# Optimization experiments

Hardware: AMD Instinct MI355X
Metric: run time of the kernel (lower is better)

The kernel has to match this reference:

```python
import jax, jax.numpy as jnp
import numpy as np

D = 64       # CNF state dimension
H = 512      # MLP hidden width
B = 8192     # batch


def setup_inputs() -> dict:
    key = jax.random.key(0)
    ks = jax.random.split(key, 8)
    s1 = 1.0 / np.sqrt(D + 1)
    s2 = 1.0 / np.sqrt(H)
    return {
        "t": jax.random.uniform(ks[0], (1,), dtype=jnp.float32),
        "x": jax.random.normal(ks[1], (B, D + 1), dtype=jnp.float32),
        "W1": jax.random.normal(ks[2], (D + 1, H), dtype=jnp.float32) * s1,
        "b1": jnp.zeros((H,), dtype=jnp.float32),
        "W2": jax.random.normal(ks[3], (H, H), dtype=jnp.float32) * s2,
        "b2": jnp.zeros((H,), dtype=jnp.float32),
        "W3": jax.random.normal(ks[4], (H, D), dtype=jnp.float32) * s2,
        "b3": jnp.zeros((D,), dtype=jnp.float32),
    }


def reference(t, x, W1, b1, W2, b2, W3, b3):
    # CNF.forward: strip log-density channel, evaluate vf and its exact divergence.
    xs = x[..., :-1]                      # [B, D]
    tt = t[0]

    def vf_single(xi):                    # xi: [D] -> [D]
        inp = jnp.concatenate([tt[None], xi])          # vf(t*ones, x) with t prepended
        h = jnp.tanh(inp @ W1 + b1)
        h = jnp.tanh(h @ W2 + b2)
        return h @ W3 + b3

    dx = jax.vmap(vf_single)(xs)                        # [B, D]
    # exact divergence: trace of per-sample Jacobian via reverse-mode (matches torch jacrev)
    J = jax.vmap(jax.jacrev(vf_single))(xs)             # [B, D, D]
    div = jnp.trace(J, axis1=-2, axis2=-1)              # [B]
    return jnp.concatenate([dx, div[:, None]], axis=-1) # [B, D+1]
```

## Files before the change

### kernel.cpp

```cpp
#include <hip/hip_runtime.h>

#define HH 512
#define DD 64
#define MROWS 16
#define TPB 256
#define LP 520

typedef unsigned short u16;
typedef short s16x8 __attribute__((ext_vector_type(8)));
typedef float f32x4 __attribute__((ext_vector_type(4)));

#define MFMA16(A,B,C) __builtin_amdgcn_mfma_f32_16x16x32_bf16((A),(B),(C),0,0,0)

#define OFF_W2K  0
#define OFF_EFK  262144
#define OFF_W1F  524288
#define OFF_W3F  557056
#define OFF_Z0B  (589824 * 2)

__device__ __forceinline__ u16 f2bf(float f) {
    unsigned u = __builtin_bit_cast(unsigned, f);
    u += 0x7fffu + ((u >> 16) & 1u);
    return (u16)(u >> 16);
}
__device__ __forceinline__ float bf2f(u16 h) {
    return __builtin_bit_cast(float, (unsigned)h << 16);
}
__device__ __forceinline__ float fast_tanh(float x) {
    float e = __expf(2.0f * x);
    return 1.0f - 2.0f * __builtin_amdgcn_rcpf(e + 1.0f);
}
__device__ __forceinline__ void gll(const u16* g, u16* l) {
    __builtin_amdgcn_global_load_lds(
        (const __attribute__((address_space(1))) unsigned int*)g,
        (__attribute__((address_space(3))) unsigned int*)l, 16, 0, 0);
}
__device__ __forceinline__ void wait_vm4() {
    asm volatile("s_waitcnt vmcnt(4)" ::: "memory");
}
__device__ __forceinline__ void wait_vm0() {
    asm volatile("s_waitcnt vmcnt(0)" ::: "memory");
}
__device__ __forceinline__ void fence_lds_reads() {
    asm volatile("s_waitcnt lgkmcnt(0)" ::: "memory");
}

__global__ __launch_bounds__(256) void precompute(
    const float* __restrict__ t,  const float* __restrict__ W1,
    const float* __restrict__ b1, const float* __restrict__ W2,
    const float* __restrict__ W3, u16* __restrict__ ws16, float* __restrict__ z0)
{
    __shared__ float T[16 * 264 > 256 * 20 ? 16 * 264 : 256 * 20];
    u16* W2K = ws16 + OFF_W2K;
    u16* EFK = ws16 + OFF_EFK;
    u16* W1F = ws16 + OFF_W1F;
    u16* W3F = ws16 + OFF_W3F;

    const int bid = blockIdx.x, tid = threadIdx.x;
    const int lane = tid & 63, wv = tid >> 6;
    const int m16 = lane & 15, q = lane >> 4;

    if (bid < 64) {
        const int nt = bid >> 1, bh = bid & 1;
        const int a0 = nt * 16, b0 = bh * 256;
        s16x8 afh[2], afl[2];
#pragma unroll
        for (int h = 0; h < 2; ++h)
#pragma unroll
            for (int j = 0; j < 8; ++j) {
                int i = h * 32 + q * 8 + j;
                float v = W1[(1 + i) * HH + a0 + m16];
                u16 hi = f2bf(v);
                afh[h][j] = (short)hi;
                afl[h][j] = (short)f2bf(v - bf2f(hi));
            }
#pragma unroll
        for (int bt = 0; bt < 4; ++bt) {
            int bl = wv * 64 + bt * 16;
            s16x8 bfh[2], bfl[2];
#pragma unroll
            for (int h = 0; h < 2; ++h) {
                const float* src = W3 + (b0 + bl + m16) * DD + h * 32 + q * 8;
                float4 p0 = *(const float4*)(src);
                float4 p1 = *(const float4*)(src + 4);
                float vv[8] = {p0.x,p0.y,p0.z,p0.w,p1.x,p1.y,p1.z,p1.w};
#pragma unroll
                for (int j = 0; j < 8; ++j) {
                    u16 hi = f2bf(vv[j]);
                    bfh[h][j] = (short)hi;
                    bfl[h][j] = (short)f2bf(vv[j] - bf2f(hi));
                }
            }
            f32x4 c = {0.f, 0.f, 0.f, 0.f};
#pragma unroll
            for (int h = 0; h < 2; ++h) {
                c = MFMA16(afh[h], bfh[h], c);
                c = MFMA16(afh[h], bfl[h], c);
                c = MFMA16(afl[h], bfh[h], c);
            }
#pragma unroll
            for (int r = 0; r < 4; ++r)
                T[(4 * q + r) * 264 + bl + m16] = c[r];
        }
        __syncthreads();
#pragma unroll
        for (int p = 0; p < 2; ++p) {
            int ksl = p * 4 + wv;
            int al  = m16;
            int blc = ksl * 32 + q * 8;
            const float* w2p = W2 + (a0 + al) * HH + b0 + blc;
            float4 wa = *(const float4*)(w2p), wb = *(const float4*)(w2p + 4);
            const float* glp = T + al * 264 + blc;
            s16x8 o;
            o[0]=(short)f2bf(wa.x*glp[0]); o[1]=(short)f2bf(wa.y*glp[1]);
            o[2]=(short)f2bf(wa.z*glp[2]); o[3]=(short)f2bf(wa.w*glp[3]);
            o[4]=(short)f2bf(wb.x*glp[4]); o[5]=(short)f2bf(wb.y*glp[5]);
            o[6]=(short)f2bf(wb.z*glp[6]); o[7]=(short)f2bf(wb.w*glp[7]);
            *(s16x8*)(EFK + (b0 / 32 + ksl) * 16384 + nt * 512 + lane * 8) = o;
        }
        if (bh == 0 && tid < 128) {
            int ks = tid >> 6, ln = tid & 63;
            int n  = nt * 16 + (ln & 15);
            int k0 = ks * 32 + (ln >> 4) * 8;
            s16x8 o;
#pragma unroll
            for (int j = 0; j < 8; ++j) o[j] = (short)f2bf(W1[(1 + k0 + j) * HH + n]);
            *(s16x8*)(W1F + nt * 1024 + ks * 512 + ln * 8) = o;
        }
    } else if (bid < 128) {
        const int nt = (bid - 64) >> 1, kh = (bid - 64) & 1;
        const int n0 = nt * 16, k0 = kh * 256;
#pragma unroll
        for (int it = 0; it < 4; ++it) {
            int r = (tid >> 2) + it * 64;
            int c = (tid & 3) * 4;
            float4 v = *(const float4*)(W2 + (k0 + r) * HH + n0 + c);
            *(float4*)(T + r * 20 + c) = v;
        }
        __syncthreads();
#pragma unroll
        for (int p = 0; p < 2; ++p) {
            int ksl = p * 4 + wv;
            int kqx = ksl * 32 + q * 8;
            s16x8 o;
#pragma unroll
            for (int j = 0; j < 8; ++j) o[j] = (short)f2bf(T[(kqx + j) * 20 + m16]);
            *(s16x8*)(W2K + (k0 / 32 + ksl) * 16384 + nt * 512 + lane * 8) = o;
        }
    } else if (bid < 136) {
        const int ot = (bid - 128) >> 1, kh = (bid - 128) & 1;
        const int o0 = ot * 16, k0 = kh * 256;
#pragma unroll
        for (int it = 0; it < 4; ++it) {
            int r = (tid >> 2) + it * 64;
            int c = (tid & 3) * 4;
            float4 v = *(const float4*)(W3 + (k0 + r) * DD + o0 + c);
            *(float4*)(T + r * 20 + c) = v;
        }
        __syncthreads();
#pragma unroll
        for (int p = 0; p < 2; ++p) {
            int ksl = p * 4 + wv;
            int kqx = ksl * 32 + q * 8;
            s16x8 o;
#pragma unroll
            for (int j = 0; j < 8; ++j) o[j] = (short)f2bf(T[(kqx + j) * 20 + m16]);
            *(s16x8*)(W3F + ot * 8192 + (k0 / 32 + ksl) * 512 + lane * 8) = o;
        }
    } else {
        for (int n = tid; n < HH; n += 256)
            z0[n] = b1[n] + t[0] * W1[n];
    }
}

__global__ __launch_bounds__(TPB) void cnf_main(
    const float* __restrict__ x,  const u16* __restrict__ ws16,
    const float* __restrict__ z0, const float* __restrict__ b2,
    const float* __restrict__ b3, float* __restrict__ out)
{
    __shared__ u16 h1s[MROWS * LP];
    __shared__ u16 h2s[MROWS * LP];
    __shared__ u16 stg[2][8192];
    __shared__ float z0s[HH];
    __shared__ float b2s[HH];
    __shared__ float b3s[DD];
    __shared__ float divacc[4][MROWS];

    const u16* W2K = ws16 + OFF_W2K;
    const u16* EFK = ws16 + OFF_EFK;
    const u16* W1F = ws16 + OFF_W1F;
    const u16* W3F = ws16 + OFF_W3F;

    const int tid  = threadIdx.x;
    const int lane = tid & 63;
    const int w    = tid >> 6;
    const int m16  = lane & 15;
    const int q    = lane >> 4;
    const int kq   = q * 8;
    const int r0   = blockIdx.x * MROWS;

    u16* xs = h2s;

    for (int idx = tid; idx < MROWS * DD; idx += TPB) {
        int r = idx >> 6, c = idx & 63;
        xs[r * 72 + c] = f2bf(x[(r0 + r) * (DD + 1) + c]);
    }
    for (int n = tid; n < HH; n += TPB) { z0s[n] = z0[n]; b2s[n] = b2[n]; }
    if (tid < DD) b3s[tid] = b3[tid];

    s16x8 b1f[8][2];
#pragma unroll
    for (int j = 0; j < 8; ++j) {
        const u16* bb = W1F + (w * 8 + j) * 1024 + lane * 8;
        b1f[j][0] = *(const s16x8*)(bb);
        b1f[j][1] = *(const s16x8*)(bb + 512);
    }
    __syncthreads();

    {
        s16x8 xa0 = *(const s16x8*)(xs + m16 * 72 + kq);
        s16x8 xa1 = *(const s16x8*)(xs + m16 * 72 + 32 + kq);
#pragma unroll
        for (int j = 0; j < 8; ++j) {
            f32x4 c = {0.f, 0.f, 0.f, 0.f};
            c = MFMA16(xa0, b1f[j][0], c);
            c = MFMA16(xa1, b1f[j][1], c);
            int col = (w * 8 + j) * 16 + m16;
#pragma unroll
            for (int i = 0; i < 4; ++i)
                h1s[(4 * q + i) * LP + col] = f2bf(fast_tanh(c[i] + z0s[col]));
        }
    }
    __syncthreads();

    {
        const u16* abase = h1s + m16 * LP + kq;
        u16* my0 = stg[0] + w * 2048;
        u16* my1 = stg[1] + w * 2048;
#pragma unroll
        for (int g = 0; g < 2; ++g) {
            const u16* wbase = W2K + (g * 16 + w * 4) * 512 + lane * 8;
            fence_lds_reads();
#pragma unroll
            for (int j = 0; j < 4; ++j) gll(wbase + j * 512,         my0 + j * 512);
#pragma unroll
            for (int j = 0; j < 4; ++j) gll(wbase + 16384 + j * 512, my1 + j * 512);
            f32x4 acc[4];
#pragma unroll
            for (int j = 0; j < 4; ++j) acc[j] = f32x4{0.f,0.f,0.f,0.f};
#pragma unroll 4
            for (int c = 0; c < 16; ++c) {
                if (c < 15) wait_vm4(); else wait_vm0();
                u16* sb = (c & 1) ? my1 : my0;
                s16x8 bf0 = *(const s16x8*)(sb +        lane * 8);
                s16x8 bf1 = *(const s16x8*)(sb +  512 + lane * 8);
                s16x8 bf2 = *(const s16x8*)(sb + 1024 + lane * 8);
                s16x8 bf3 = *(const s16x8*)(sb + 1536 + lane * 8);
                s16x8 af  = *(const s16x8*)(abase + c * 32);
                acc[0] = MFMA16(af, bf0, acc[0]);
                acc[1] = MFMA16(af, bf1, acc[1]);
                acc[2] = MFMA16(af, bf2, acc[2]);
                acc[3] = MFMA16(af, bf3, acc[3]);
                if (c < 14) {
                    fence_lds_reads();
                    const u16* src = wbase + (c + 2) * 16384;
#pragma unroll
                    for (int j = 0; j < 4; ++j) gll(src + j * 512, sb + j * 512);
                }
            }
#pragma unroll
            for (int j = 0; j < 4; ++j) {
                int col = (g * 16 + w * 4 + j) * 16 + m16;
#pragma unroll
                for (int i = 0; i < 4; ++i)
                    h2s[(4 * q + i) * LP + col] = f2bf(fast_tanh(acc[j][i] + b2s[col]));
            }
        }
    }
    __syncthreads();

    {
        const u16* ap = h2s + m16 * LP + kq;
        const u16* bp = W3F + w * 8192 + lane * 8;
        s16x8 W3r[4];
#pragma unroll
        for (int k = 0; k < 4; ++k) W3r[k] = *(const s16x8*)(bp + k * 512);
        f32x4 cA = {0.f,0.f,0.f,0.f}, cB = {0.f,0.f,0.f,0.f};
#pragma unroll
        for (int c = 0; c < 16; ++c) {
            s16x8 f = *(const s16x8*)(ap + c * 32);
            const int sl = c & 3;
            if (c & 1) cB = MFMA16(f, W3r[sl], cB);
            else       cA = MFMA16(f, W3r[sl], cA);
            if (c < 12) W3r[sl] = *(const s16x8*)(bp + (c + 4) * 512);
        }
        f32x4 c3 = cA + cB;
        int o = w * 16 + m16;
#pragma unroll
        for (int i = 0; i < 4; ++i)
            out[(r0 + 4 * q + i) * (DD + 1) + o] = c3[i] + b3s[o];
    }

    {
        const u16* abase = h2s + m16 * LP + kq;
        u16* my0 = stg[0] + w * 2048;
        u16* my1 = stg[1] + w * 2048;
        float dpart[4] = {0.f, 0.f, 0.f, 0.f};
#pragma unroll
        for (int g = 0; g < 2; ++g) {
            const u16* ebase = EFK + (g * 16 + w * 4) * 512 + lane * 8;
            fence_lds_reads();
#pragma unroll
            for (int j = 0; j < 4; ++j) gll(ebase + j * 512,         my0 + j * 512);
#pragma unroll
            for (int j = 0; j < 4; ++j) gll(ebase + 16384 + j * 512, my1 + j * 512);
            f32x4 acc[4];
#pragma unroll
            for (int j = 0; j < 4; ++j) acc[j] = f32x4{0.f,0.f,0.f,0.f};
#pragma unroll 4
            for (int c = 0; c < 16; ++c) {
                if (c < 15) wait_vm4(); else wait_vm0();
                u16* sb = (c & 1) ? my1 : my0;
                s16x8 bf0 = *(const s16x8*)(sb +        lane * 8);
                s16x8 bf1 = *(const s16x8*)(sb +  512 + lane * 8);
                s16x8 bf2 = *(const s16x8*)(sb + 1024 + lane * 8);
                s16x8 bf3 = *(const s16x8*)(sb + 1536 + lane * 8);
                s16x8 hf  = *(const s16x8*)(abase + c * 32);
                s16x8 af;
#pragma unroll
                for (int jj = 0; jj < 8; ++jj) {
                    float f = bf2f((u16)hf[jj]);
                    af[jj] = (short)f2bf(1.0f - f * f);
                }
                acc[0] = MFMA16(af, bf0, acc[0]);
                acc[1] = MFMA16(af, bf1, acc[1]);
                acc[2] = MFMA16(af, bf2, acc[2]);
                acc[3] = MFMA16(af, bf3, acc[3]);
                if (c < 14) {
                    fence_lds_reads();
                    const u16* src = ebase + (c + 2) * 16384;
#pragma unroll
                    for (int j = 0; j < 4; ++j) gll(src + j * 512, sb + j * 512);
                }
            }
#pragma unroll
            for (int j = 0; j < 4; ++j) {
                int col = (g * 16 + w * 4 + j) * 16 + m16;
#pragma unroll
                for (int i = 0; i < 4; ++i) {
                    float h1v = bf2f(h1s[(4 * q + i) * LP + col]);
                    dpart[i] += (1.0f - h1v * h1v) * acc[j][i];
                }
            }
        }
#pragma unroll
        for (int i = 0; i < 4; ++i) {
            float v = dpart[i];
            v += __shfl_xor(v, 1, 64);
            v += __shfl_xor(v, 2, 64);
            v += __shfl_xor(v, 4, 64);
            v += __shfl_xor(v, 8, 64);
            if (m16 == 0) divacc[w][4 * q + i] = v;
        }
    }
    __syncthreads();

    if (tid < MROWS) {
        float s = divacc[0][tid] + divacc[1][tid] + divacc[2][tid] + divacc[3][tid];
        out[(r0 + tid) * (DD + 1) + DD] = s;
    }
}

extern "C" void kernel_launch(void* const* d_in, const int* in_sizes, int n_in,
                              void* d_out, int out_size, void* d_ws, size_t ws_size,
                              hipStream_t stream) {
    const float* t  = (const float*)d_in[0];
    const float* x  = (const float*)d_in[1];
    const float* W1 = (const float*)d_in[2];
    const float* b1 = (const float*)d_in[3];
    const float* W2 = (const float*)d_in[4];
    const float* b2 = (const float*)d_in[5];
    const float* W3 = (const float*)d_in[6];
    const float* b3 = (const float*)d_in[7];
    float* out = (float*)d_out;

    u16*   ws16 = (u16*)d_ws;
    float* z0   = (float*)((char*)d_ws + OFF_Z0B);

    precompute<<<137, 256, 0, stream>>>(t, W1, b1, W2, W3, ws16, z0);
    cnf_main<<<8192 / MROWS, TPB, 0, stream>>>(x, ws16, z0, b2, b3, out);
}
```

Before: 104.3 us.

## Process 32 rows per block with 8 waves sharing staged weight tiles

Doubles rows per block to 32 and threads to 512, so each staged W2/EF weight tile feeds two row-tiles of MFMAs. The per-block loop over two column groups goes away, which halves global weight traffic per row. The first W2 tile prefetch is issued before the input load, and the EF prefetch is started before the layer-2 epilogue. The layer-1 tanh derivative is now kept in registers instead of re-read from LDS. In exchange LDS use per block and register pressure both grow, and there are half as many blocks.

```diff
diff --git a/kernel.cpp b/kernel.cpp
--- a/kernel.cpp
+++ b/kernel.cpp
@@ -2,8 +2,8 @@
 
 #define HH 512
 #define DD 64
-#define MROWS 16
-#define TPB 256
+#define MROWS 32
+#define TPB 512
 #define LP 520
 
 typedef unsigned short u16;
@@ -180,11 +180,11 @@
 {
     __shared__ u16 h1s[MROWS * LP];
     __shared__ u16 h2s[MROWS * LP];
-    __shared__ u16 stg[2][8192];
+    __shared__ u16 stg[2][16384];
     __shared__ float z0s[HH];
     __shared__ float b2s[HH];
     __shared__ float b3s[DD];
-    __shared__ float divacc[4][MROWS];
+    __shared__ float divacc[8][MROWS];
 
     const u16* W2K = ws16 + OFF_W2K;
     const u16* EFK = ws16 + OFF_EFK;
@@ -201,87 +201,117 @@
 
     u16* xs = h2s;
 
+#pragma unroll
+    for (int j = 0; j < 4; ++j)
+        gll(W2K + (4 * w + j) * 512 + lane * 8,         stg[0] + w * 2048 + j * 512);
+#pragma unroll
+    for (int j = 0; j < 4; ++j)
+        gll(W2K + 16384 + (4 * w + j) * 512 + lane * 8, stg[1] + w * 2048 + j * 512);
+
     for (int idx = tid; idx < MROWS * DD; idx += TPB) {
         int r = idx >> 6, c = idx & 63;
         xs[r * 72 + c] = f2bf(x[(r0 + r) * (DD + 1) + c]);
     }
-    for (int n = tid; n < HH; n += TPB) { z0s[n] = z0[n]; b2s[n] = b2[n]; }
+    z0s[tid] = z0[tid];
+    b2s[tid] = b2[tid];
     if (tid < DD) b3s[tid] = b3[tid];
 
-    s16x8 b1f[8][2];
-#pragma unroll
-    for (int j = 0; j < 8; ++j) {
-        const u16* bb = W1F + (w * 8 + j) * 1024 + lane * 8;
+    s16x8 b1f[4][2];
+#pragma unroll
+    for (int j = 0; j < 4; ++j) {
+        const u16* bb = W1F + (4 * w + j) * 1024 + lane * 8;
         b1f[j][0] = *(const s16x8*)(bb);
         b1f[j][1] = *(const s16x8*)(bb + 512);
     }
     __syncthreads();
 
+    float d1reg[2][4][4];
+
     {
-        s16x8 xa0 = *(const s16x8*)(xs + m16 * 72 + kq);
-        s16x8 xa1 = *(const s16x8*)(xs + m16 * 72 + 32 + kq);
-#pragma unroll
-        for (int j = 0; j < 8; ++j) {
-            f32x4 c = {0.f, 0.f, 0.f, 0.f};
-            c = MFMA16(xa0, b1f[j][0], c);
-            c = MFMA16(xa1, b1f[j][1], c);
-            int col = (w * 8 + j) * 16 + m16;
+        s16x8 xa[2][2];
+#pragma unroll
+        for (int rt = 0; rt < 2; ++rt) {
+            xa[rt][0] = *(const s16x8*)(xs + (rt * 16 + m16) * 72 + kq);
+            xa[rt][1] = *(const s16x8*)(xs + (rt * 16 + m16) * 72 + 32 + kq);
+        }
+#pragma unroll
+        for (int j = 0; j < 4; ++j) {
+            int col = (4 * w + j) * 16 + m16;
+#pragma unroll
+            for (int rt = 0; rt < 2; ++rt) {
+                f32x4 c = {0.f, 0.f, 0.f, 0.f};
+                c = MFMA16(xa[rt][0], b1f[j][0], c);
+                c = MFMA16(xa[rt][1], b1f[j][1], c);
+#pragma unroll
+                for (int i = 0; i < 4; ++i) {
+                    float hv = fast_tanh(c[i] + z0s[col]);
+                    h1s[(rt * 16 + 4 * q + i) * LP + col] = f2bf(hv);
+                    d1reg[rt][j][i] = 1.0f - hv * hv;
+                }
+            }
+        }
+    }
+    __syncthreads();
+
+    f32x4 acc[2][4];
+#pragma unroll
+    for (int rt = 0; rt < 2; ++rt)
+#pragma unroll
+        for (int j = 0; j < 4; ++j) acc[rt][j] = f32x4{0.f,0.f,0.f,0.f};
+    {
+        const u16* ap0 = h1s + m16 * LP + kq;
+        const u16* ap1 = h1s + (16 + m16) * LP + kq;
+#pragma unroll 4
+        for (int c = 0; c < 16; ++c) {
+            if (c < 15) wait_vm4(); else wait_vm0();
+            u16* sb = stg[c & 1] + w * 2048;
+            s16x8 bf0 = *(const s16x8*)(sb +        lane * 8);
+            s16x8 bf1 = *(const s16x8*)(sb +  512 + lane * 8);
+            s16x8 bf2 = *(const s16x8*)(sb + 1024 + lane * 8);
+            s16x8 bf3 = *(const s16x8*)(sb + 1536 + lane * 8);
+            s16x8 f0  = *(const s16x8*)(ap0 + c * 32);
+            s16x8 f1  = *(const s16x8*)(ap1 + c * 32);
+            acc[0][0] = MFMA16(f0, bf0, acc[0][0]);
+            acc[1][0] = MFMA16(f1, bf0, acc[1][0]);
+            acc[0][1] = MFMA16(f0, bf1, acc[0][1]);
+            acc[1][1] = MFMA16(f1, bf1, acc[1][1]);
+            acc[0][2] = MFMA16(f0, bf2, acc[0][2]);
+            acc[1][2] = MFMA16(f1, bf2, acc[1][2]);
+            acc[0][3] = MFMA16(f0, bf3, acc[0][3]);
+            acc[1][3] = MFMA16(f1, bf3, acc[1][3]);
+            if (c < 14) {
+                fence_lds_reads();
+                const u16* src = W2K + (c + 2) * 16384 + 4 * w * 512 + lane * 8;
+#pragma unroll
+                for (int j = 0; j < 4; ++j) gll(src + j * 512, sb + j * 512);
+            }
+        }
+    }
+
+    fence_lds_reads();
+#pragma unroll
+    for (int j = 0; j < 4; ++j)
+        gll(EFK + (4 * w + j) * 512 + lane * 8,         stg[0] + w * 2048 + j * 512);
+#pragma unroll
+    for (int j = 0; j < 4; ++j)
+        gll(EFK + 16384 + (4 * w + j) * 512 + lane * 8, stg[1] + w * 2048 + j * 512);
+
+#pragma unroll
+    for (int j = 0; j < 4; ++j) {
+        int col = (4 * w + j) * 16 + m16;
+#pragma unroll
+        for (int rt = 0; rt < 2; ++rt)
 #pragma unroll
             for (int i = 0; i < 4; ++i)
-                h1s[(4 * q + i) * LP + col] = f2bf(fast_tanh(c[i] + z0s[col]));
-        }
+                h2s[(rt * 16 + 4 * q + i) * LP + col] =
+                    f2bf(fast_tanh(acc[rt][j][i] + b2s[col]));
     }
     __syncthreads();
 
     {
-        const u16* abase = h1s + m16 * LP + kq;
-        u16* my0 = stg[0] + w * 2048;
-        u16* my1 = stg[1] + w * 2048;
-#pragma unroll
-        for (int g = 0; g < 2; ++g) {
-            const u16* wbase = W2K + (g * 16 + w * 4) * 512 + lane * 8;
-            fence_lds_reads();
-#pragma unroll
-            for (int j = 0; j < 4; ++j) gll(wbase + j * 512,         my0 + j * 512);
-#pragma unroll
-            for (int j = 0; j < 4; ++j) gll(wbase + 16384 + j * 512, my1 + j * 512);
-            f32x4 acc[4];
-#pragma unroll
-            for (int j = 0; j < 4; ++j) acc[j] = f32x4{0.f,0.f,0.f,0.f};
-#pragma unroll 4
-            for (int c = 0; c < 16; ++c) {
-                if (c < 15) wait_vm4(); else wait_vm0();
-                u16* sb = (c & 1) ? my1 : my0;
-                s16x8 bf0 = *(const s16x8*)(sb +        lane * 8);
-                s16x8 bf1 = *(const s16x8*)(sb +  512 + lane * 8);
-                s16x8 bf2 = *(const s16x8*)(sb + 1024 + lane * 8);
-                s16x8 bf3 = *(const s16x8*)(sb + 1536 + lane * 8);
-                s16x8 af  = *(const s16x8*)(abase + c * 32);
-                acc[0] = MFMA16(af, bf0, acc[0]);
-                acc[1] = MFMA16(af, bf1, acc[1]);
-                acc[2] = MFMA16(af, bf2, acc[2]);
-                acc[3] = MFMA16(af, bf3, acc[3]);
-                if (c < 14) {
-                    fence_lds_reads();
-                    const u16* src = wbase + (c + 2) * 16384;
-#pragma unroll
-                    for (int j = 0; j < 4; ++j) gll(src + j * 512, sb + j * 512);
-                }
-            }
-#pragma unroll
-            for (int j = 0; j < 4; ++j) {
-                int col = (g * 16 + w * 4 + j) * 16 + m16;
-#pragma unroll
-                for (int i = 0; i < 4; ++i)
-                    h2s[(4 * q + i) * LP + col] = f2bf(fast_tanh(acc[j][i] + b2s[col]));
-            }
-        }
-    }
-    __syncthreads();
-
-    {
-        const u16* ap = h2s + m16 * LP + kq;
-        const u16* bp = W3F + w * 8192 + lane * 8;
+        const int rowt = w >> 2, ot = w & 3;
+        const u16* ap = h2s + (rowt * 16 + m16) * LP + kq;
+        const u16* bp = W3F + ot * 8192 + lane * 8;
         s16x8 W3r[4];
 #pragma unroll
         for (int k = 0; k < 4; ++k) W3r[k] = *(const s16x8*)(bp + k * 512);
@@ -295,78 +325,74 @@
             if (c < 12) W3r[sl] = *(const s16x8*)(bp + (c + 4) * 512);
         }
         f32x4 c3 = cA + cB;
-        int o = w * 16 + m16;
+        int o = ot * 16 + m16;
 #pragma unroll
         for (int i = 0; i < 4; ++i)
-            out[(r0 + 4 * q + i) * (DD + 1) + o] = c3[i] + b3s[o];
+            out[(r0 + rowt * 16 + 4 * q + i) * (DD + 1) + o] = c3[i] + b3s[o];
     }
 
     {
-        const u16* abase = h2s + m16 * LP + kq;
-        u16* my0 = stg[0] + w * 2048;
-        u16* my1 = stg[1] + w * 2048;
-        float dpart[4] = {0.f, 0.f, 0.f, 0.f};
-#pragma unroll
-        for (int g = 0; g < 2; ++g) {
-            const u16* ebase = EFK + (g * 16 + w * 4) * 512 + lane * 8;
-            fence_lds_reads();
-#pragma unroll
-            for (int j = 0; j < 4; ++j) gll(ebase + j * 512,         my0 + j * 512);
-#pragma unroll
-            for (int j = 0; j < 4; ++j) gll(ebase + 16384 + j * 512, my1 + j * 512);
-            f32x4 acc[4];
-#pragma unroll
-            for (int j = 0; j < 4; ++j) acc[j] = f32x4{0.f,0.f,0.f,0.f};
+        f32x4 g[2][4];
+#pragma unroll
+        for (int rt = 0; rt < 2; ++rt)
+#pragma unroll
+            for (int j = 0; j < 4; ++j) g[rt][j] = f32x4{0.f,0.f,0.f,0.f};
+        const u16* ap0 = h2s + m16 * LP + kq;
+        const u16* ap1 = h2s + (16 + m16) * LP + kq;
 #pragma unroll 4
-            for (int c = 0; c < 16; ++c) {
-                if (c < 15) wait_vm4(); else wait_vm0();
-                u16* sb = (c & 1) ? my1 : my0;
-                s16x8 bf0 = *(const s16x8*)(sb +        lane * 8);
-                s16x8 bf1 = *(const s16x8*)(sb +  512 + lane * 8);
-                s16x8 bf2 = *(const s16x8*)(sb + 1024 + lane * 8);
-                s16x8 bf3 = *(const s16x8*)(sb + 1536 + lane * 8);
-                s16x8 hf  = *(const s16x8*)(abase + c * 32);
-                s16x8 af;
-#pragma unroll
-                for (int jj = 0; jj < 8; ++jj) {
-                    float f = bf2f((u16)hf[jj]);
-                    af[jj] = (short)f2bf(1.0f - f * f);
-                }
-                acc[0] = MFMA16(af, bf0, acc[0]);
-                acc[1] = MFMA16(af, bf1, acc[1]);
-                acc[2] = MFMA16(af, bf2, acc[2]);
-                acc[3] = MFMA16(af, bf3, acc[3]);
-                if (c < 14) {
-                    fence_lds_reads();
-                    const u16* src = ebase + (c + 2) * 16384;
-#pragma unroll
-                    for (int j = 0; j < 4; ++j) gll(src + j * 512, sb + j * 512);
-                }
-            }
-#pragma unroll
-            for (int j = 0; j < 4; ++j) {
-                int col = (g * 16 + w * 4 + j) * 16 + m16;
-#pragma unroll
-                for (int i = 0; i < 4; ++i) {
-                    float h1v = bf2f(h1s[(4 * q + i) * LP + col]);
-                    dpart[i] += (1.0f - h1v * h1v) * acc[j][i];
-                }
-            }
-        }
-#pragma unroll
-        for (int i = 0; i < 4; ++i) {
-            float v = dpart[i];
-            v += __shfl_xor(v, 1, 64);
-            v += __shfl_xor(v, 2, 64);
-            v += __shfl_xor(v, 4, 64);
-            v += __shfl_xor(v, 8, 64);
-            if (m16 == 0) divacc[w][4 * q + i] = v;
-        }
+        for (int c = 0; c < 16; ++c) {
+            if (c < 15) wait_vm4(); else wait_vm0();
+            u16* sb = stg[c & 1] + w * 2048;
+            s16x8 ef0 = *(const s16x8*)(sb +        lane * 8);
+            s16x8 ef1 = *(const s16x8*)(sb +  512 + lane * 8);
+            s16x8 ef2 = *(const s16x8*)(sb + 1024 + lane * 8);
+            s16x8 ef3 = *(const s16x8*)(sb + 1536 + lane * 8);
+            s16x8 hf0 = *(const s16x8*)(ap0 + c * 32);
+            s16x8 hf1 = *(const s16x8*)(ap1 + c * 32);
+            s16x8 af0, af1;
+#pragma unroll
+            for (int jj = 0; jj < 8; ++jj) {
+                float v0 = bf2f((u16)hf0[jj]);
+                float v1 = bf2f((u16)hf1[jj]);
+                af0[jj] = (short)f2bf(1.0f - v0 * v0);
+                af1[jj] = (short)f2bf(1.0f - v1 * v1);
+            }
+            g[0][0] = MFMA16(af0, ef0, g[0][0]);
+            g[1][0] = MFMA16(af1, ef0, g[1][0]);
+            g[0][1] = MFMA16(af0, ef1, g[0][1]);
+            g[1][1] = MFMA16(af1, ef1, g[1][1]);
+            g[0][2] = MFMA16(af0, ef2, g[0][2]);
+            g[1][2] = MFMA16(af1, ef2, g[1][2]);
+            g[0][3] = MFMA16(af0, ef3, g[0][3]);
+            g[1][3] = MFMA16(af1, ef3, g[1][3]);
+            if (c < 14) {
+                fence_lds_reads();
+                const u16* src = EFK + (c + 2) * 16384 + 4 * w * 512 + lane * 8;
+#pragma unroll
+                for (int j = 0; j < 4; ++j) gll(src + j * 512, sb + j * 512);
+            }
+        }
+#pragma unroll
+        for (int rt = 0; rt < 2; ++rt)
+#pragma unroll
+            for (int i = 0; i < 4; ++i) {
+                float v = d1reg[rt][0][i] * g[rt][0][i]
+                        + d1reg[rt][1][i] * g[rt][1][i]
+                        + d1reg[rt][2][i] * g[rt][2][i]
+                        + d1reg[rt][3][i] * g[rt][3][i];
+                v += __shfl_xor(v, 1, 64);
+                v += __shfl_xor(v, 2, 64);
+                v += __shfl_xor(v, 4, 64);
+                v += __shfl_xor(v, 8, 64);
+                if (m16 == 0) divacc[w][rt * 16 + 4 * q + i] = v;
+            }
     }
     __syncthreads();
 
     if (tid < MROWS) {
-        float s = divacc[0][tid] + divacc[1][tid] + divacc[2][tid] + divacc[3][tid];
+        float s = 0.0f;
+#pragma unroll
+        for (int ww = 0; ww < 8; ++ww) s += divacc[ww][tid];
         out[(r0 + tid) * (DD + 1) + DD] = s;
     }
 }
```

After: 96.82 us. 1.08x faster.
